# Optimization experiments

Hardware: AMD Instinct MI355X
Metric: run time of the kernel (lower is better)

The kernel has to match this reference:

```python
import jax, jax.numpy as jnp
import numpy as np

EPS = 1e-5

def _conv1x1(x, w, b):
    # x: [B,C,H,W], w: [O,C], b: [O] -> [B,O,H,W]
    return jnp.einsum('bchw,oc->bohw', x, w) + b[None, :, None, None]

def setup_inputs() -> dict:
    key = jax.random.key(0)
    ks = jax.random.split(key, 13)
    B, C, H, W = 16, 256, 64, 64
    Ci = C // 2
    s = 0.05
    return {
        'x': jax.random.normal(ks[0], (B, C, H, W), jnp.float32),
        'g_w': jax.random.normal(ks[1], (Ci, C), jnp.float32) * s,
        'g_b': jax.random.normal(ks[2], (Ci,), jnp.float32) * s,
        'theta_w': jax.random.normal(ks[3], (Ci, C), jnp.float32) * s,
        'theta_b': jax.random.normal(ks[4], (Ci,), jnp.float32) * s,
        'phi_w': jax.random.normal(ks[5], (Ci, C), jnp.float32) * s,
        'phi_b': jax.random.normal(ks[6], (Ci,), jnp.float32) * s,
        'w_w': jax.random.normal(ks[7], (C, Ci), jnp.float32) * s,
        'w_b': jax.random.normal(ks[8], (C,), jnp.float32) * s,
        'bn_gamma': jax.random.normal(ks[9], (C,), jnp.float32),
        'bn_beta': jax.random.normal(ks[10], (C,), jnp.float32),
        'bn_mean': jax.random.normal(ks[11], (C,), jnp.float32),
        'bn_var': jax.random.uniform(ks[12], (C,), jnp.float32, 0.5, 1.5),
    }

def reference(x, g_w, g_b, theta_w, theta_b, phi_w, phi_b,
              w_w, w_b, bn_gamma, bn_beta, bn_mean, bn_var):
    B, C, H, W = x.shape
    N = H * W
    Ci = g_w.shape[0]
    # 1x1 conv projections, flatten spatial to N
    g_x = _conv1x1(x, g_w, g_b).reshape(B, Ci, N).transpose(0, 2, 1)        # [B,N,Ci]
    theta_x = _conv1x1(x, theta_w, theta_b).reshape(B, Ci, N).transpose(0, 2, 1)  # [B,N,Ci]
    phi_x = _conv1x1(x, phi_w, phi_b).reshape(B, Ci, N)                     # [B,Ci,N]
    # affinity f = theta @ phi, normalized by N (softmax-free linear attention)
    f_div_C = jnp.einsum('bnc,bcm->bnm', theta_x, phi_x) / N                # [B,N,N]
    y = jnp.einsum('bnm,bmc->bnc', f_div_C, g_x)                            # [B,N,Ci]
    y = y.transpose(0, 2, 1).reshape(B, Ci, H, W)
    # W: 1x1 conv + BatchNorm (eval mode, running stats)
    w_y = _conv1x1(y, w_w, w_b)
    inv = bn_gamma * jax.lax.rsqrt(bn_var + EPS)
    w_y = w_y * inv[None, :, None, None] + (bn_beta - bn_mean * inv)[None, :, None, None]
    return w_y + x
```

## Files before the change

### kernel.cpp

```cpp
#include <hip/hip_runtime.h>
#include <stdint.h>

#define BATCH 16
#define CH    256
#define CI    128
#define NSP   4096
#define KC    8
#define EPSV  1e-5f

typedef unsigned short u16;
typedef __attribute__((ext_vector_type(4))) float f32x4;
typedef __attribute__((ext_vector_type(8))) short bf16x8;

__device__ __forceinline__ u16 f2b(float f) {
  uint32_t u = __float_as_uint(f);
  uint32_t r = u + 0x7FFFu + ((u >> 16) & 1u);
  return (u16)(r >> 16);
}

__device__ __forceinline__ void async16(void* lds, const void* g) {
  __builtin_amdgcn_global_load_lds(
      (const __attribute__((address_space(1))) unsigned int*)g,
      (__attribute__((address_space(3))) unsigned int*)lds, 16, 0, 0);
}

__global__ __launch_bounds__(256) void k_const(const float* __restrict__ w_w,
    const float* __restrict__ g_w, const float* __restrict__ g_b,
    const float* __restrict__ theta_w, const float* __restrict__ theta_b,
    const float* __restrict__ phi_w, const float* __restrict__ phi_b,
    const float* __restrict__ w_b, const float* __restrict__ bn_g,
    const float* __restrict__ bn_b, const float* __restrict__ bn_m,
    const float* __restrict__ bn_v,
    float* __restrict__ E, float* __restrict__ KT, float* __restrict__ wg,
    float* __restrict__ tphi, float* __restrict__ q, float* __restrict__ inv,
    float* __restrict__ dconst, float* __restrict__ tb) {
  __shared__ float lbuf[1024];
  const int blk = blockIdx.x, t = threadIdx.x;
  if (blk < 32) {
    const int o0 = blk*8;
    #pragma unroll
    for (int k = 0; k < 4; ++k) { int idx = k*256 + t;
      lbuf[idx] = w_w[(size_t)(o0 + (idx & 7))*CI + (idx >> 3)]; }
    __syncthreads();
    float acc[8] = {0.f};
    for (int j = 0; j < CI; ++j) {
      float gv = g_w[(size_t)j*CH + t];
      #pragma unroll
      for (int r = 0; r < 8; ++r) acc[r] += lbuf[j*8 + r] * gv;
    }
    #pragma unroll
    for (int r = 0; r < 8; ++r) E[(size_t)(o0 + r)*CH + t] = acc[r];
  } else if (blk < 64) {
    const int a0 = (blk - 32)*8;
    #pragma unroll
    for (int k = 0; k < 4; ++k) { int idx = k*256 + t;
      lbuf[idx] = phi_w[(size_t)(idx >> 3)*CH + a0 + (idx & 7)]; }
    __syncthreads();
    float acc[8] = {0.f};
    for (int i = 0; i < CI; ++i) {
      float tv = theta_w[(size_t)i*CH + t];
      #pragma unroll
      for (int u = 0; u < 8; ++u) acc[u] += lbuf[i*8 + u] * tv;
    }
    #pragma unroll
    for (int u = 0; u < 8; ++u) KT[(size_t)(a0 + u)*CH + t] = acc[u];
  } else {
    float iv = bn_g[t] * rsqrtf(bn_v[t] + EPSV);
    inv[t] = iv;
    dconst[t] = iv*w_b[t] + bn_b[t] - bn_m[t]*iv;
    float a = 0.f;
    for (int j = 0; j < CI; ++j) a += w_w[(size_t)t*CI + j] * g_b[j];
    wg[t] = a;
    float tp = 0.f, qq = 0.f;
    for (int i = 0; i < CI; ++i) {
      tp += theta_w[(size_t)i*CH + t] * phi_b[i];
      qq += phi_w[(size_t)i*CH + t] * theta_b[i];
    }
    tphi[t] = tp; q[t] = qq;
    lbuf[t] = (t < CI) ? theta_b[t]*phi_b[t] : 0.f;
    __syncthreads();
    for (int s2 = 128; s2 > 0; s2 >>= 1) { if (t < s2) lbuf[t] += lbuf[t + s2]; __syncthreads(); }
    if (t == 0) tb[0] = lbuf[0];
  }
}

__global__ __launch_bounds__(256) void k_prep(const float* __restrict__ x,
    u16* __restrict__ xb, u16* __restrict__ xt, float* __restrict__ psum) {
  __shared__ float tile[64*64];
  const int b = blockIdx.z, c0 = blockIdx.y*64, n0 = blockIdx.x*64;
  const int t = threadIdx.x;
  const int lane16 = t & 15;
  const int grp = t >> 4;
  const float* xp = x + ((size_t)b*CH + c0)*NSP + n0;
  u16* xbp = xb + ((size_t)b*CH + c0)*NSP + n0;
  #pragma unroll
  for (int p = 0; p < 4; ++p) {
    int cl = grp + p*16;
    int nl = lane16*4;
    float4 v = *(const float4*)(xp + (size_t)cl*NSP + nl);
    float ps = v.x + v.y + v.z + v.w;
    #pragma unroll
    for (int o = 1; o < 16; o <<= 1) ps += __shfl_xor(ps, o, 64);
    if (lane16 == 0) psum[((size_t)b*64 + blockIdx.x)*CH + c0 + cl] = ps;
    ushort4 bv; bv.x=f2b(v.x); bv.y=f2b(v.y); bv.z=f2b(v.z); bv.w=f2b(v.w);
    *(ushort4*)(xbp + (size_t)cl*NSP + nl) = bv;
    float vv[4] = {v.x, v.y, v.z, v.w};
    #pragma unroll
    for (int j = 0; j < 4; ++j) {
      int n = nl + j;
      tile[n*64 + (cl ^ (((n>>2)&7)<<2))] = vv[j];
    }
  }
  __syncthreads();
  u16* xtp = xt + ((size_t)b*NSP + n0)*CH + c0;
  #pragma unroll
  for (int q2 = 0; q2 < 4; ++q2) {
    int nl = grp + q2*16;
    int c4 = lane16*4;
    float4 v = *(const float4*)&tile[nl*64 + (c4 ^ (((nl>>2)&7)<<2))];
    ushort4 bv; bv.x=f2b(v.x); bv.y=f2b(v.y); bv.z=f2b(v.z); bv.w=f2b(v.w);
    *(ushort4*)(xtp + (size_t)nl*CH + c4) = bv;
  }
}

__global__ __launch_bounds__(256) void k_gram(const u16* __restrict__ xb, float* __restrict__ Sp) {
  __shared__ u16 As[128*64];
  __shared__ u16 Bs[128*64];
  const int L = blockIdx.x;
  const int wk = (L & 7) * 48 + (L >> 3);
  const int b = wk / 24;
  const int rem = wk % 24;
  const int kc = rem / 3;
  const int q = rem % 3;
  const int m_base = (q == 2) ? 128 : 0;
  const int n_base = (q == 0) ? 0 : 128;
  const int t = threadIdx.x, wv = t >> 6, l = t & 63;
  const int wr = wv >> 1, wc = wv & 1;
  const int lr = l & 15, lkb = l >> 4;
  const int sr = l >> 3, ss = l & 7;
  const u16* xa = xb + (size_t)b*CH*NSP;
  const int kbeg = kc * (NSP/KC);
  f32x4 acc[4][4];
  #pragma unroll
  for (int i = 0; i < 4; ++i)
    #pragma unroll
    for (int j = 0; j < 4; ++j) acc[i][j] = (f32x4){0.f,0.f,0.f,0.f};

  for (int kk = 0; kk < 8; ++kk) {
    const int kpos = kbeg + kk*64;
    #pragma unroll
    for (int j4 = 0; j4 < 4; ++j4) {
      const int j = wv*4 + j4;
      const int r = j*8 + sr;
      async16(&As[j*512], xa + (size_t)(m_base + r)*NSP + kpos + ((ss ^ (r & 7)) * 8));
    }
    if (q == 1) {
      #pragma unroll
      for (int j4 = 0; j4 < 4; ++j4) {
        const int j = wv*4 + j4;
        const int r = j*8 + sr;
        async16(&Bs[j*512], xa + (size_t)(n_base + r)*NSP + kpos + ((ss ^ (r & 7)) * 8));
      }
    }
    __syncthreads();
    const u16* bsrc = (q == 1) ? Bs : As;
    #pragma unroll
    for (int ks = 0; ks < 2; ++ks) {
      bf16x8 A[4], Bf[4];
      #pragma unroll
      for (int mt = 0; mt < 4; ++mt) {
        const int ra = wr*64 + mt*16 + lr;
        A[mt] = *(const bf16x8*)(As + ra*64 + (((ks*4 + lkb) ^ (ra & 7)) * 8));
      }
      #pragma unroll
      for (int nt = 0; nt < 4; ++nt) {
        const int rb = wc*64 + nt*16 + lr;
        Bf[nt] = *(const bf16x8*)(bsrc + rb*64 + (((ks*4 + lkb) ^ (rb & 7)) * 8));
      }
      #pragma unroll
      for (int mt = 0; mt < 4; ++mt)
        #pragma unroll
        for (int nt = 0; nt < 4; ++nt)
          acc[mt][nt] = __builtin_amdgcn_mfma_f32_16x16x32_bf16(A[mt], Bf[nt], acc[mt][nt], 0, 0, 0);
    }
    __syncthreads();
  }
  float* Sb = Sp + (size_t)(b*KC + kc)*CH*CH;
  const int r0 = (l >> 4) * 4;
  #pragma unroll
  for (int mt = 0; mt < 4; ++mt)
    #pragma unroll
    for (int nt = 0; nt < 4; ++nt)
      #pragma unroll
      for (int rr = 0; rr < 4; ++rr)
        Sb[(size_t)(m_base + wr*64 + mt*16 + r0 + rr)*CH + n_base + wc*64 + nt*16 + lr]
          = acc[mt][nt][rr];
}

__global__ __launch_bounds__(256) void k_red(const float* __restrict__ Sp, float* __restrict__ S) {
  __shared__ float tl[64*65];
  const int b = blockIdx.y, tt = blockIdx.x, t = threadIdx.x;
  const int qq = tt >> 2, sub = tt & 3;
  const int qi = (qq == 2) ? 1 : 0, qj = (qq == 0) ? 0 : 1;
  const int row0 = qi*128 + (sub >> 1)*64, col0 = qj*128 + (sub & 1)*64;
  const float* p = Sp + (size_t)b*KC*CH*CH;
  float* Sb = S + (size_t)b*CH*CH;
  float4 sum[4];
  #pragma unroll
  for (int k = 0; k < 4; ++k) {
    const int slot = t + k*256;
    const int r = slot >> 4, c4 = (slot & 15) * 4;
    float4 s = {0.f,0.f,0.f,0.f};
    #pragma unroll
    for (int kc = 0; kc < KC; ++kc) {
      float4 v = *(const float4*)(p + (size_t)kc*CH*CH + (size_t)(row0 + r)*CH + col0 + c4);
      s.x += v.x; s.y += v.y; s.z += v.z; s.w += v.w;
    }
    sum[k] = s;
    *(float4*)(Sb + (size_t)(row0 + r)*CH + col0 + c4) = s;
  }
  if (qq == 1) {
    #pragma unroll
    for (int k = 0; k < 4; ++k) {
      const int slot = t + k*256;
      const int r = slot >> 4, c4 = (slot & 15) * 4;
      tl[r*65 + c4+0] = sum[k].x; tl[r*65 + c4+1] = sum[k].y;
      tl[r*65 + c4+2] = sum[k].z; tl[r*65 + c4+3] = sum[k].w;
    }
    __syncthreads();
    #pragma unroll
    for (int k = 0; k < 4; ++k) {
      const int slot = t + k*256;
      const int r = slot >> 4, c4 = (slot & 15) * 4;
      float4 v = { tl[(c4+0)*65 + r], tl[(c4+1)*65 + r], tl[(c4+2)*65 + r], tl[(c4+3)*65 + r] };
      *(float4*)(Sb + (size_t)(col0 + r)*CH + row0 + c4) = v;
    }
  }
}

__global__ __launch_bounds__(256) void k_vec2(const float* __restrict__ psum,
    const float* __restrict__ E, const float* __restrict__ KT,
    const float* __restrict__ q, float* __restrict__ KS, float* __restrict__ Es,
    float* __restrict__ qs) {
  __shared__ float ls[CH];
  __shared__ float rbuf[4];
  const int b = blockIdx.x, t = threadIdx.x;
  float s = 0.f;
  for (int xb = 0; xb < 64; ++xb) s += psum[((size_t)b*64 + xb)*CH + t];
  ls[t] = s;
  __syncthreads();
  float ks = 0.f;
  for (int a = 0; a < CH; ++a) ks += KT[(size_t)a*CH + t] * ls[a];
  KS[(size_t)b*CH + t] = ks;
  float es = 0.f;
  for (int c = 0; c < CH; ++c) es += E[(size_t)t*CH + c] * ls[c];
  Es[(size_t)b*CH + t] = es;
  float p = q[t] * ls[t];
  #pragma unroll
  for (int o = 1; o < 64; o <<= 1) p += __shfl_xor(p, o, 64);
  if ((t & 63) == 0) rbuf[t >> 6] = p;
  __syncthreads();
  if (t == 0) qs[b] = rbuf[0] + rbuf[1] + rbuf[2] + rbuf[3];
}

__global__ __launch_bounds__(256) void k_RP(const float* __restrict__ S,
    const float* __restrict__ E, const float* __restrict__ KT,
    const float* __restrict__ q, const float* __restrict__ KS,
    const float* __restrict__ Es, const float* __restrict__ qs,
    const float* __restrict__ wg, const float* __restrict__ tphi,
    const float* __restrict__ inv, const float* __restrict__ dconst,
    const float* __restrict__ tb, u16* __restrict__ Pb, float* __restrict__ dv) {
  __shared__ float lEt[2048];
  __shared__ float lRt[2048];
  __shared__ float red[32];
  const int b = blockIdx.y, o0 = blockIdx.x*8, t = threadIdx.x;
  #pragma unroll
  for (int k = 0; k < 8; ++k) { int idx = k*256 + t;
    lEt[idx] = E[(size_t)(o0 + (idx & 7))*CH + (idx >> 3)]; }
  __syncthreads();
  const float* Sb = S + (size_t)b*CH*CH;
  float acc[8] = {0.f};
  for (int c = 0; c < CH; ++c) {
    float sv = Sb[(size_t)c*CH + t];
    #pragma unroll
    for (int r = 0; r < 8; ++r) acc[r] += lEt[c*8 + r] * sv;
  }
  #pragma unroll
  for (int r = 0; r < 8; ++r) lRt[t*8 + r] = acc[r];
  const float qt = q[t];
  #pragma unroll
  for (int r = 0; r < 8; ++r) {
    float p = acc[r] * qt;
    #pragma unroll
    for (int o = 1; o < 64; o <<= 1) p += __shfl_xor(p, o, 64);
    if ((t & 63) == 0) red[r*4 + (t >> 6)] = p;
  }
  __syncthreads();
  float acc2[8] = {0.f};
  for (int a = 0; a < CH; ++a) {
    float kv = KT[(size_t)a*CH + t];
    #pragma unroll
    for (int r = 0; r < 8; ++r) acc2[r] += lRt[a*8 + r] * kv;
  }
  const float ksv = KS[(size_t)b*CH + t], tpv = tphi[t];
  u16* Pbb = Pb + (size_t)b*CH*CH;
  #pragma unroll
  for (int r = 0; r < 8; ++r) {
    int o = o0 + r;
    float val = (acc2[r] + wg[o]*ksv + (Es[(size_t)b*CH + o] + (float)NSP*wg[o])*tpv)
                * inv[o] * (1.f/(float)NSP);
    if (o == t) val += 1.f;
    Pbb[(size_t)o*CH + t] = f2b(val);
  }
  if (t < 8) {
    int o = o0 + t;
    float iv = inv[o], wgo = wg[o], tb0 = tb[0];
    float rq = red[t*4] + red[t*4+1] + red[t*4+2] + red[t*4+3];
    float t2 = rq + wgo*qs[b] + Es[(size_t)b*CH + o]*tb0;
    dv[(size_t)b*CH + o] = iv*(t2*(1.f/(float)NSP) + wgo*tb0) + dconst[o];
  }
}

__global__ __launch_bounds__(512, 4) void k_apply(const u16* __restrict__ Pb,
    const u16* __restrict__ xt, const float* __restrict__ dv,
    float* __restrict__ out) {
  __shared__ union {
    u16   bx[64*256];
    float fe[8][16][68];
  } sm;
  const int b = blockIdx.y, n0 = blockIdx.x*64;
  const int t = threadIdx.x, w = t >> 6, l = t & 63;
  {
    const u16* src = xt + ((size_t)b*NSP + n0)*CH;
    const int r = t >> 3, sbase = t & 7;
    #pragma unroll
    for (int it = 0; it < 4; ++it) {
      int slot = sbase + it*8;
      bf16x8 v = *(const bf16x8*)(src + (size_t)r*CH + slot*8);
      *(bf16x8*)(sm.bx + r*256 + ((slot ^ (r & 7)) * 8)) = v;
    }
  }
  __syncthreads();
  const int m0 = w*32;
  const int lr = l & 15, lkb = l >> 4;
  const int sw = lr & 7;
  const u16* Pp = Pb + (size_t)b*CH*CH;
  f32x4 acc[2][4];
  #pragma unroll
  for (int i = 0; i < 2; ++i)
    #pragma unroll
    for (int j = 0; j < 4; ++j) acc[i][j] = (f32x4){0.f,0.f,0.f,0.f};
  #pragma unroll
  for (int kk = 0; kk < 8; ++kk) {
    bf16x8 A[2], Bf[4];
    #pragma unroll
    for (int mt = 0; mt < 2; ++mt)
      A[mt] = *(const bf16x8*)(Pp + (size_t)(m0 + mt*16 + lr)*CH + kk*32 + lkb*8);
    #pragma unroll
    for (int nt = 0; nt < 4; ++nt) {
      int slot = kk*4 + lkb;
      Bf[nt] = *(const bf16x8*)(sm.bx + (nt*16 + lr)*256 + ((slot ^ sw) * 8));
    }
    #pragma unroll
    for (int mt = 0; mt < 2; ++mt)
      #pragma unroll
      for (int nt = 0; nt < 4; ++nt)
        acc[mt][nt] = __builtin_amdgcn_mfma_f32_16x16x32_bf16(A[mt], Bf[nt], acc[mt][nt], 0, 0, 0);
  }
  __syncthreads();
  float* ob = out + (size_t)b*CH*NSP;
  const int r0 = (l >> 4) * 4;
  #pragma unroll
  for (int mt = 0; mt < 2; ++mt) {
    #pragma unroll
    for (int rr = 0; rr < 4; ++rr) {
      float dval = dv[(size_t)b*CH + m0 + mt*16 + r0 + rr];
      #pragma unroll
      for (int nt = 0; nt < 4; ++nt)
        sm.fe[w][r0 + rr][nt*16 + lr] = acc[mt][nt][rr] + dval;
    }
    #pragma unroll
    for (int i = 0; i < 4; ++i) {
      int s = l + 64*i;
      int rrow = s >> 4, c4 = (s & 15) * 4;
      float4 v = *(const float4*)&sm.fe[w][rrow][c4];
      *(float4*)&ob[(size_t)(m0 + mt*16 + rrow)*NSP + n0 + c4] = v;
    }
  }
}

static constexpr size_t XT_OFF = 0;
static constexpr size_t S_OFF  = 33554432;
static constexpr size_t PB_OFF = 37748736;
static constexpr size_t PS_OFF = 39845888;
static constexpr size_t E_OFF  = 40894464;
static constexpr size_t KT_OFF = 41156608;
static constexpr size_t WG_OFF = 41418752;
static constexpr size_t TP_OFF = 41419776;
static constexpr size_t QV_OFF = 41420800;
static constexpr size_t IV_OFF = 41421824;
static constexpr size_t DC_OFF = 41422848;
static constexpr size_t TB_OFF = 41423872;
static constexpr size_t KS_OFF = 41424896;
static constexpr size_t ES_OFF = 41441280;
static constexpr size_t QS_OFF = 41457664;
static constexpr size_t DV_OFF = 41458688;

extern "C" void kernel_launch(void* const* d_in, const int* in_sizes, int n_in,
                              void* d_out, int out_size, void* d_ws, size_t ws_size,
                              hipStream_t stream) {
  const float* x       = (const float*)d_in[0];
  const float* g_w     = (const float*)d_in[1];
  const float* g_b     = (const float*)d_in[2];
  const float* theta_w = (const float*)d_in[3];
  const float* theta_b = (const float*)d_in[4];
  const float* phi_w   = (const float*)d_in[5];
  const float* phi_b   = (const float*)d_in[6];
  const float* w_w     = (const float*)d_in[7];
  const float* w_b     = (const float*)d_in[8];
  const float* bn_g    = (const float*)d_in[9];
  const float* bn_b    = (const float*)d_in[10];
  const float* bn_m    = (const float*)d_in[11];
  const float* bn_v    = (const float*)d_in[12];
  float* out = (float*)d_out;
  char* ws = (char*)d_ws;
  u16*   XT = (u16*)(ws + XT_OFF);
  float* S  = (float*)(ws + S_OFF);
  u16*   Pb = (u16*)(ws + PB_OFF);
  float* PS = (float*)(ws + PS_OFF);
  float* E  = (float*)(ws + E_OFF);
  float* KT = (float*)(ws + KT_OFF);
  float* WG = (float*)(ws + WG_OFF);
  float* TP = (float*)(ws + TP_OFF);
  float* QV = (float*)(ws + QV_OFF);
  float* IV = (float*)(ws + IV_OFF);
  float* DC = (float*)(ws + DC_OFF);
  float* TB = (float*)(ws + TB_OFF);
  float* KS = (float*)(ws + KS_OFF);
  float* ES = (float*)(ws + ES_OFF);
  float* QS = (float*)(ws + QS_OFF);
  float* DV = (float*)(ws + DV_OFF);
  u16*   Xb = (u16*)d_out;
  float* Sp = (float*)((char*)d_out + 33554432);

  k_const<<<dim3(65),                    256, 0, stream>>>(w_w, g_w, g_b, theta_w, theta_b,
                                                           phi_w, phi_b, w_b, bn_g, bn_b, bn_m, bn_v,
                                                           E, KT, WG, TP, QV, IV, DC, TB);
  k_prep <<<dim3(NSP/64, CH/64, BATCH),  256, 0, stream>>>(x, Xb, XT, PS);
  k_gram <<<dim3(384),                   256, 0, stream>>>(Xb, Sp);
  k_red  <<<dim3(12, BATCH),             256, 0, stream>>>(Sp, S);
  k_vec2 <<<dim3(BATCH),                 256, 0, stream>>>(PS, E, KT, QV, KS, ES, QS);
  k_RP   <<<dim3(32, BATCH),             256, 0, stream>>>(S, E, KT, QV, KS, ES, QS, WG, TP, IV, DC, TB, Pb, DV);
  k_apply<<<dim3(NSP/64, BATCH),         512, 0, stream>>>(Pb, XT, DV, out);
}
```

Baseline: 131.2 us.

## Use 64x64 symmetric Gram tiles with fewer K-chunks and fuse reduction with vector kernel

The Gram computation now uses 64x64 output tiles over the 10 upper-triangular blocks instead of three 128x128 quadrants, with the K split reduced from 8 to 4 chunks. This gives 640 blocks, which should balance the work across CUs better and shrink the partial-sum buffer. The separate reduction and vector kernels are merged into one launch, saving a kernel launch. The trade-off is less operand reuse per block, since each block runs 4 MFMAs per k-step instead of 16, plus more LDS barrier steps per block.

```diff
diff --git a/kernel.cpp b/kernel.cpp
--- a/kernel.cpp
+++ b/kernel.cpp
@@ -5,7 +5,7 @@
 #define CH    256
 #define CI    128
 #define NSP   4096
-#define KC    8
+#define KC    4
 #define EPSV  1e-5f
 
 typedef unsigned short u16;
@@ -124,143 +124,148 @@
 }
 
 __global__ __launch_bounds__(256) void k_gram(const u16* __restrict__ xb, float* __restrict__ Sp) {
-  __shared__ u16 As[128*64];
-  __shared__ u16 Bs[128*64];
+  __shared__ u16 As[64*64];
+  __shared__ u16 Bs[64*64];
+  const int TIa[10] = {0,0,0,0,1,1,1,2,2,3};
+  const int TJa[10] = {0,1,2,3,1,2,3,2,3,3};
   const int L = blockIdx.x;
-  const int wk = (L & 7) * 48 + (L >> 3);
-  const int b = wk / 24;
-  const int rem = wk % 24;
-  const int kc = rem / 3;
-  const int q = rem % 3;
-  const int m_base = (q == 2) ? 128 : 0;
-  const int n_base = (q == 0) ? 0 : 128;
+  const int wk = (L & 7) * 80 + (L >> 3);
+  const int b = wk / 40;
+  const int rem = wk % 40;
+  const int kc = rem / 10;
+  const int tile = rem % 10;
+  const int ti = TIa[tile], tj = TJa[tile];
+  const int m_base = ti*64, n_base = tj*64;
+  const bool diag = (ti == tj);
   const int t = threadIdx.x, wv = t >> 6, l = t & 63;
   const int wr = wv >> 1, wc = wv & 1;
   const int lr = l & 15, lkb = l >> 4;
-  const int sr = l >> 3, ss = l & 7;
+  const int sr8 = l >> 3, ss = l & 7;
   const u16* xa = xb + (size_t)b*CH*NSP;
   const int kbeg = kc * (NSP/KC);
-  f32x4 acc[4][4];
-  #pragma unroll
-  for (int i = 0; i < 4; ++i)
-    #pragma unroll
-    for (int j = 0; j < 4; ++j) acc[i][j] = (f32x4){0.f,0.f,0.f,0.f};
-
-  for (int kk = 0; kk < 8; ++kk) {
+  f32x4 acc[2][2];
+  #pragma unroll
+  for (int i = 0; i < 2; ++i)
+    #pragma unroll
+    for (int j = 0; j < 2; ++j) acc[i][j] = (f32x4){0.f,0.f,0.f,0.f};
+
+  for (int kk = 0; kk < 16; ++kk) {
     const int kpos = kbeg + kk*64;
     #pragma unroll
-    for (int j4 = 0; j4 < 4; ++j4) {
-      const int j = wv*4 + j4;
-      const int r = j*8 + sr;
-      async16(&As[j*512], xa + (size_t)(m_base + r)*NSP + kpos + ((ss ^ (r & 7)) * 8));
-    }
-    if (q == 1) {
-      #pragma unroll
-      for (int j4 = 0; j4 < 4; ++j4) {
-        const int j = wv*4 + j4;
-        const int r = j*8 + sr;
-        async16(&Bs[j*512], xa + (size_t)(n_base + r)*NSP + kpos + ((ss ^ (r & 7)) * 8));
-      }
-    }
-    __syncthreads();
-    const u16* bsrc = (q == 1) ? Bs : As;
+    for (int j = 0; j < 2; ++j) {
+      const int g = wv*2 + j;
+      const int r = g*8 + sr8;
+      async16(&As[g*512], xa + (size_t)(m_base + r)*NSP + kpos + ((ss ^ (r & 7)) * 8));
+    }
+    if (!diag) {
+      #pragma unroll
+      for (int j = 0; j < 2; ++j) {
+        const int g = wv*2 + j;
+        const int r = g*8 + sr8;
+        async16(&Bs[g*512], xa + (size_t)(n_base + r)*NSP + kpos + ((ss ^ (r & 7)) * 8));
+      }
+    }
+    __syncthreads();
+    const u16* bsrc = diag ? As : Bs;
     #pragma unroll
     for (int ks = 0; ks < 2; ++ks) {
-      bf16x8 A[4], Bf[4];
-      #pragma unroll
-      for (int mt = 0; mt < 4; ++mt) {
-        const int ra = wr*64 + mt*16 + lr;
+      bf16x8 A[2], Bf[2];
+      #pragma unroll
+      for (int mt = 0; mt < 2; ++mt) {
+        const int ra = wr*32 + mt*16 + lr;
         A[mt] = *(const bf16x8*)(As + ra*64 + (((ks*4 + lkb) ^ (ra & 7)) * 8));
       }
       #pragma unroll
-      for (int nt = 0; nt < 4; ++nt) {
-        const int rb = wc*64 + nt*16 + lr;
+      for (int nt = 0; nt < 2; ++nt) {
+        const int rb = wc*32 + nt*16 + lr;
         Bf[nt] = *(const bf16x8*)(bsrc + rb*64 + (((ks*4 + lkb) ^ (rb & 7)) * 8));
       }
       #pragma unroll
-      for (int mt = 0; mt < 4; ++mt)
+      for (int mt = 0; mt < 2; ++mt)
         #pragma unroll
-        for (int nt = 0; nt < 4; ++nt)
+        for (int nt = 0; nt < 2; ++nt)
           acc[mt][nt] = __builtin_amdgcn_mfma_f32_16x16x32_bf16(A[mt], Bf[nt], acc[mt][nt], 0, 0, 0);
     }
     __syncthreads();
   }
-  float* Sb = Sp + (size_t)(b*KC + kc)*CH*CH;
+  float* Sb = Sp + (size_t)((b*KC + kc)*10 + tile)*4096;
   const int r0 = (l >> 4) * 4;
   #pragma unroll
-  for (int mt = 0; mt < 4; ++mt)
-    #pragma unroll
-    for (int nt = 0; nt < 4; ++nt)
-      #pragma unroll
-      for (int rr = 0; rr < 4; ++rr)
-        Sb[(size_t)(m_base + wr*64 + mt*16 + r0 + rr)*CH + n_base + wc*64 + nt*16 + lr]
-          = acc[mt][nt][rr];
-}
-
-__global__ __launch_bounds__(256) void k_red(const float* __restrict__ Sp, float* __restrict__ S) {
-  __shared__ float tl[64*65];
-  const int b = blockIdx.y, tt = blockIdx.x, t = threadIdx.x;
-  const int qq = tt >> 2, sub = tt & 3;
-  const int qi = (qq == 2) ? 1 : 0, qj = (qq == 0) ? 0 : 1;
-  const int row0 = qi*128 + (sub >> 1)*64, col0 = qj*128 + (sub & 1)*64;
-  const float* p = Sp + (size_t)b*KC*CH*CH;
-  float* Sb = S + (size_t)b*CH*CH;
-  float4 sum[4];
-  #pragma unroll
-  for (int k = 0; k < 4; ++k) {
-    const int slot = t + k*256;
-    const int r = slot >> 4, c4 = (slot & 15) * 4;
-    float4 s = {0.f,0.f,0.f,0.f};
-    #pragma unroll
-    for (int kc = 0; kc < KC; ++kc) {
-      float4 v = *(const float4*)(p + (size_t)kc*CH*CH + (size_t)(row0 + r)*CH + col0 + c4);
-      s.x += v.x; s.y += v.y; s.z += v.z; s.w += v.w;
-    }
-    sum[k] = s;
-    *(float4*)(Sb + (size_t)(row0 + r)*CH + col0 + c4) = s;
-  }
-  if (qq == 1) {
+  for (int mt = 0; mt < 2; ++mt)
+    #pragma unroll
+    for (int nt = 0; nt < 2; ++nt)
+      #pragma unroll
+      for (int rr = 0; rr < 4; ++rr) {
+        const int lm = wr*32 + mt*16 + r0 + rr;
+        const int lc = wc*32 + nt*16 + lr;
+        Sb[lm*64 + lc] = acc[mt][nt][rr];
+      }
+}
+
+__global__ __launch_bounds__(256) void k_redvec(const float* __restrict__ Sp,
+    const float* __restrict__ psum, const float* __restrict__ E,
+    const float* __restrict__ KT, const float* __restrict__ q,
+    float* __restrict__ S, float* __restrict__ KS, float* __restrict__ Es,
+    float* __restrict__ qs) {
+  __shared__ float tl[64*65 + 8];
+  const int b = blockIdx.y, xx = blockIdx.x, t = threadIdx.x;
+  if (xx < 10) {
+    const int TIa[10] = {0,0,0,0,1,1,1,2,2,3};
+    const int TJa[10] = {0,1,2,3,1,2,3,2,3,3};
+    const int ti = TIa[xx], tj = TJa[xx];
+    const int row0 = ti*64, col0 = tj*64;
+    float* Sb = S + (size_t)b*CH*CH;
+    float4 sum[4];
     #pragma unroll
     for (int k = 0; k < 4; ++k) {
       const int slot = t + k*256;
       const int r = slot >> 4, c4 = (slot & 15) * 4;
-      tl[r*65 + c4+0] = sum[k].x; tl[r*65 + c4+1] = sum[k].y;
-      tl[r*65 + c4+2] = sum[k].z; tl[r*65 + c4+3] = sum[k].w;
-    }
-    __syncthreads();
-    #pragma unroll
-    for (int k = 0; k < 4; ++k) {
-      const int slot = t + k*256;
-      const int r = slot >> 4, c4 = (slot & 15) * 4;
-      float4 v = { tl[(c4+0)*65 + r], tl[(c4+1)*65 + r], tl[(c4+2)*65 + r], tl[(c4+3)*65 + r] };
-      *(float4*)(Sb + (size_t)(col0 + r)*CH + row0 + c4) = v;
-    }
-  }
-}
-
-__global__ __launch_bounds__(256) void k_vec2(const float* __restrict__ psum,
-    const float* __restrict__ E, const float* __restrict__ KT,
-    const float* __restrict__ q, float* __restrict__ KS, float* __restrict__ Es,
-    float* __restrict__ qs) {
-  __shared__ float ls[CH];
-  __shared__ float rbuf[4];
-  const int b = blockIdx.x, t = threadIdx.x;
-  float s = 0.f;
-  for (int xb = 0; xb < 64; ++xb) s += psum[((size_t)b*64 + xb)*CH + t];
-  ls[t] = s;
-  __syncthreads();
-  float ks = 0.f;
-  for (int a = 0; a < CH; ++a) ks += KT[(size_t)a*CH + t] * ls[a];
-  KS[(size_t)b*CH + t] = ks;
-  float es = 0.f;
-  for (int c = 0; c < CH; ++c) es += E[(size_t)t*CH + c] * ls[c];
-  Es[(size_t)b*CH + t] = es;
-  float p = q[t] * ls[t];
-  #pragma unroll
-  for (int o = 1; o < 64; o <<= 1) p += __shfl_xor(p, o, 64);
-  if ((t & 63) == 0) rbuf[t >> 6] = p;
-  __syncthreads();
-  if (t == 0) qs[b] = rbuf[0] + rbuf[1] + rbuf[2] + rbuf[3];
+      float4 s = {0.f,0.f,0.f,0.f};
+      #pragma unroll
+      for (int kc = 0; kc < KC; ++kc) {
+        const float* p = Sp + (size_t)((b*KC + kc)*10 + xx)*4096;
+        float4 v = *(const float4*)(p + r*64 + c4);
+        s.x += v.x; s.y += v.y; s.z += v.z; s.w += v.w;
+      }
+      sum[k] = s;
+      *(float4*)(Sb + (size_t)(row0 + r)*CH + col0 + c4) = s;
+    }
+    if (ti != tj) {
+      #pragma unroll
+      for (int k = 0; k < 4; ++k) {
+        const int slot = t + k*256;
+        const int r = slot >> 4, c4 = (slot & 15) * 4;
+        tl[r*65 + c4+0] = sum[k].x; tl[r*65 + c4+1] = sum[k].y;
+        tl[r*65 + c4+2] = sum[k].z; tl[r*65 + c4+3] = sum[k].w;
+      }
+      __syncthreads();
+      #pragma unroll
+      for (int k = 0; k < 4; ++k) {
+        const int slot = t + k*256;
+        const int r = slot >> 4, c4 = (slot & 15) * 4;
+        float4 v = { tl[(c4+0)*65 + r], tl[(c4+1)*65 + r],
+                     tl[(c4+2)*65 + r], tl[(c4+3)*65 + r] };
+        *(float4*)(Sb + (size_t)(col0 + r)*CH + row0 + c4) = v;
+      }
+    }
+  } else {
+    float s = 0.f;
+    for (int nb = 0; nb < 64; ++nb) s += psum[((size_t)b*64 + nb)*CH + t];
+    tl[t] = s;
+    __syncthreads();
+    float ks = 0.f;
+    for (int a = 0; a < CH; ++a) ks += KT[(size_t)a*CH + t] * tl[a];
+    KS[(size_t)b*CH + t] = ks;
+    float es = 0.f;
+    for (int c = 0; c < CH; ++c) es += E[(size_t)t*CH + c] * tl[c];
+    Es[(size_t)b*CH + t] = es;
+    float p = q[t] * tl[t];
+    #pragma unroll
+    for (int o = 1; o < 64; o <<= 1) p += __shfl_xor(p, o, 64);
+    if ((t & 63) == 0) tl[4160 + (t >> 6)] = p;
+    __syncthreads();
+    if (t == 0) qs[b] = tl[4160] + tl[4161] + tl[4162] + tl[4163];
+  }
 }
 
 __global__ __launch_bounds__(256) void k_RP(const float* __restrict__ S,
@@ -443,13 +448,12 @@
   u16*   Xb = (u16*)d_out;
   float* Sp = (float*)((char*)d_out + 33554432);
 
-  k_const<<<dim3(65),                    256, 0, stream>>>(w_w, g_w, g_b, theta_w, theta_b,
-                                                           phi_w, phi_b, w_b, bn_g, bn_b, bn_m, bn_v,
-                                                           E, KT, WG, TP, QV, IV, DC, TB);
-  k_prep <<<dim3(NSP/64, CH/64, BATCH),  256, 0, stream>>>(x, Xb, XT, PS);
-  k_gram <<<dim3(384),                   256, 0, stream>>>(Xb, Sp);
-  k_red  <<<dim3(12, BATCH),             256, 0, stream>>>(Sp, S);
-  k_vec2 <<<dim3(BATCH),                 256, 0, stream>>>(PS, E, KT, QV, KS, ES, QS);
-  k_RP   <<<dim3(32, BATCH),             256, 0, stream>>>(S, E, KT, QV, KS, ES, QS, WG, TP, IV, DC, TB, Pb, DV);
-  k_apply<<<dim3(NSP/64, BATCH),         512, 0, stream>>>(Pb, XT, DV, out);
-}
+  k_const <<<dim3(65),                    256, 0, stream>>>(w_w, g_w, g_b, theta_w, theta_b,
+                                                            phi_w, phi_b, w_b, bn_g, bn_b, bn_m, bn_v,
+                                                            E, KT, WG, TP, QV, IV, DC, TB);
+  k_prep  <<<dim3(NSP/64, CH/64, BATCH),  256, 0, stream>>>(x, Xb, XT, PS);
+  k_gram  <<<dim3(640),                   256, 0, stream>>>(Xb, Sp);
+  k_redvec<<<dim3(11, BATCH),             256, 0, stream>>>(Sp, PS, E, KT, QV, S, KS, ES, QS);
+  k_RP    <<<dim3(32, BATCH),             256, 0, stream>>>(S, E, KT, QV, KS, ES, QS, WG, TP, IV, DC, TB, Pb, DV);
+  k_apply <<<dim3(NSP/64, BATCH),         512, 0, stream>>>(Pb, XT, DV, out);
+}
```

Result: faster. 127.3 us (-3.0%).
